# Performance work log

Hardware: AMD Instinct MI355X
Metric: run time of the kernel (lower is better)

Reference implementation:

```python
import jax, jax.numpy as jnp
import numpy as np

VOCAB, EMB, HID, B, T = 32000, 256, 256, 64, 2048


def setup_inputs() -> dict:
    key = jax.random.key(0)
    ks = jax.random.split(key, 6)
    s = 1.0 / np.sqrt(HID)
    return {
        "source": jax.random.randint(ks[0], (B, T), 0, VOCAB),
        "embedding": jax.random.normal(ks[1], (VOCAB, EMB), dtype=jnp.float32) * 0.02,
        "W_ih": jax.random.uniform(ks[2], (EMB, HID), jnp.float32, -s, s),
        "W_hh": jax.random.uniform(ks[3], (HID, HID), jnp.float32, -s, s),
        "b_ih": jax.random.uniform(ks[4], (HID,), jnp.float32, -s, s),
        "b_hh": jax.random.uniform(ks[5], (HID,), jnp.float32, -s, s),
    }


def reference(source, embedding, W_ih, W_hh, b_ih, b_hh):
    # embedding lookup: [B, T, EMB]
    embedded = embedding[source]
    # scan over time with carried hidden state (RNNCellManual: tanh cell)
    xs = jnp.swapaxes(embedded, 0, 1)  # [T, B, EMB]

    def step(h, x_t):
        h_new = jnp.tanh(x_t @ W_ih + b_ih + h @ W_hh + b_hh)
        return h_new, None

    h0 = jnp.zeros((source.shape[0], W_hh.shape[0]), dtype=embedding.dtype)
    h_T, _ = jax.lax.scan(step, h0, xs)
    return h_T  # final hidden state [B, HID]
```

## Files before the change

### kernel.cpp

```cpp
#include <hip/hip_runtime.h>

#define TT 2048
#define BB 64
#define HH 256

typedef _Float16 half2_t __attribute__((ext_vector_type(2)));
typedef _Float16 half8_t __attribute__((ext_vector_type(8)));
typedef float f32x4 __attribute__((ext_vector_type(4)));
typedef int i32x4 __attribute__((ext_vector_type(4)));

__global__ void prep_kernel(const float* __restrict__ Wih, const float* __restrict__ Whh,
                            _Float16* __restrict__ WihT, _Float16* __restrict__ WhhT) {
  const int n = blockIdx.x;
  const int k = threadIdx.x;
  WihT[n * HH + k] = (_Float16)Wih[k * HH + n];
  WhhT[n * HH + k] = (_Float16)Whh[k * HH + n];
}

__global__ __launch_bounds__(256, 2) void embed_gemm_kernel(
    const int* __restrict__ source, const float* __restrict__ emb,
    const _Float16* __restrict__ WihT, const float* __restrict__ b_ih,
    const float* __restrict__ b_hh, _Float16* __restrict__ U) {
  const int t = blockIdx.x;
  const int nbase = blockIdx.y * 64;
  __shared__ __align__(16) _Float16 Bs[64][280];

  const int tid = threadIdx.x;
  for (int c = tid; c < 64 * 32; c += 256) {
    const int n = c >> 5;
    const int ko = (c & 31) * 8;
    *(half8_t*)&Bs[n][ko] = *(const half8_t*)(WihT + (size_t)(nbase + n) * HH + ko);
  }
  __syncthreads();

  const int lane = tid & 63;
  const int wave = tid >> 6;
  const int row16 = lane & 15;
  const int quad = lane >> 4;
  const int b = wave * 16 + row16;
  const int src = source[b * TT + t];
  const float* arow = emb + (size_t)src * HH + quad * 8;

  f32x4 acc[4];
#pragma unroll
  for (int ct = 0; ct < 4; ++ct) acc[ct] = (f32x4){0.f, 0.f, 0.f, 0.f};

#pragma unroll
  for (int kt = 0; kt < 8; ++kt) {
    const float4 x0 = *(const float4*)(arow + kt * 32);
    const float4 x1 = *(const float4*)(arow + kt * 32 + 4);
    half8_t af;
    af[0] = (_Float16)x0.x; af[1] = (_Float16)x0.y;
    af[2] = (_Float16)x0.z; af[3] = (_Float16)x0.w;
    af[4] = (_Float16)x1.x; af[5] = (_Float16)x1.y;
    af[6] = (_Float16)x1.z; af[7] = (_Float16)x1.w;
#pragma unroll
    for (int ct = 0; ct < 4; ++ct) {
      const half8_t bf = *(const half8_t*)&Bs[ct * 16 + row16][quad * 8 + kt * 32];
      acc[ct] = __builtin_amdgcn_mfma_f32_16x16x32_f16(af, bf, acc[ct], 0, 0, 0);
    }
  }

#pragma unroll
  for (int ct = 0; ct < 4; ++ct) {
    const int nn = nbase + ct * 16 + row16;
    const float bias = b_ih[nn] + b_hh[nn];
#pragma unroll
    for (int r = 0; r < 4; ++r) {
      const int bb = wave * 16 + quad * 4 + r;
      U[((size_t)t * BB + bb) * HH + nn] = (_Float16)(acc[ct][r] + bias);
    }
  }
}

__global__ __launch_bounds__(256)
__attribute__((amdgpu_waves_per_eu(1, 1)))
void rnn_scan_kernel(
    const _Float16* __restrict__ U, const _Float16* __restrict__ WhhT,
    float* __restrict__ out) {
  const int b = blockIdx.x;
  const int tid = threadIdx.x;
  const int w = tid >> 6;
  const int l = tid & 63;
  const int col = l & 15;
  const int quad = l >> 4;

  __shared__ __align__(16) _Float16 hbuf[2][HH];

  half8_t wb[4][8];
#pragma unroll
  for (int tt = 0; tt < 4; ++tt) {
    const _Float16* base = WhhT + (size_t)(64 * w + 16 * tt + col) * HH + quad * 8;
#pragma unroll
    for (int c = 0; c < 8; ++c) wb[tt][c] = *(const half8_t*)(base + 32 * c);
  }
  asm volatile("" : "+a"(wb[0][0]), "+a"(wb[0][1]), "+a"(wb[0][2]), "+a"(wb[0][3]),
                    "+a"(wb[0][4]), "+a"(wb[0][5]), "+a"(wb[0][6]), "+a"(wb[0][7]),
                    "+a"(wb[1][0]), "+a"(wb[1][1]), "+a"(wb[1][2]), "+a"(wb[1][3]),
                    "+a"(wb[1][4]), "+a"(wb[1][5]), "+a"(wb[1][6]), "+a"(wb[1][7]));
  asm volatile("" : "+a"(wb[2][0]), "+a"(wb[2][1]), "+a"(wb[2][2]), "+a"(wb[2][3]),
                    "+a"(wb[2][4]), "+a"(wb[2][5]), "+a"(wb[2][6]), "+a"(wb[2][7]),
                    "+a"(wb[3][0]), "+a"(wb[3][1]), "+a"(wb[3][2]), "+a"(wb[3][3]),
                    "+a"(wb[3][4]), "+a"(wb[3][5]), "+a"(wb[3][6]), "+a"(wb[3][7]));

  hbuf[0][tid] = (_Float16)0.f;

  const _Float16* Up = U + b * HH + tid;
  _Float16 uc[8], un[8];
#pragma unroll
  for (int s = 0; s < 8; ++s) uc[s] = Up[(size_t)s * (BB * HH)];

  float hn = 0.f;
  __syncthreads();

  for (int tc = 0; tc < TT; tc += 8) {
    const int tn = (tc + 8) & (TT - 1);
#pragma unroll
    for (int s = 0; s < 8; ++s) un[s] = Up[(size_t)(tn + s) * (BB * HH)];

#pragma unroll
    for (int s = 0; s < 8; ++s) {
      const int t = tc + s;

      const _Float16* hrow = hbuf[t & 1] + quad * 8;
      half8_t ha[8];
#pragma unroll
      for (int c = 0; c < 8; ++c) ha[c] = *(const half8_t*)(hrow + 32 * c);
      asm volatile("" : "+v"(ha[0]), "+v"(ha[1]), "+v"(ha[2]), "+v"(ha[3]),
                        "+v"(ha[4]), "+v"(ha[5]), "+v"(ha[6]), "+v"(ha[7]));

      f32x4 cacc[4];
#pragma unroll
      for (int tt = 0; tt < 4; ++tt) cacc[tt] = (f32x4){0.f, 0.f, 0.f, 0.f};
#pragma unroll
      for (int c = 0; c < 8; ++c)
#pragma unroll
        for (int tt = 0; tt < 4; ++tt)
          cacc[tt] = __builtin_amdgcn_mfma_f32_16x16x32_f16(ha[c], wb[tt][c], cacc[tt], 0, 0, 0);

      float y = cacc[0][0];
      y = (quad == 1) ? cacc[1][0] : y;
      y = (quad == 2) ? cacc[2][0] : y;
      y = (quad == 3) ? cacc[3][0] : y;

      const float a = (float)uc[s] + y;
      const float e = __builtin_amdgcn_exp2f(a * 2.885390081777927f);
      hn = 1.f - 2.f * __builtin_amdgcn_rcpf(e + 1.f);
      hbuf[(t + 1) & 1][tid] = (_Float16)hn;

      __syncthreads();
    }
#pragma unroll
    for (int s = 0; s < 8; ++s) uc[s] = un[s];
  }
  out[(size_t)b * HH + tid] = hn;
}

extern "C" void kernel_launch(void* const* d_in, const int* in_sizes, int n_in,
                              void* d_out, int out_size, void* d_ws, size_t ws_size,
                              hipStream_t stream) {
  const int*   source = (const int*)d_in[0];
  const float* emb    = (const float*)d_in[1];
  const float* Wih    = (const float*)d_in[2];
  const float* Whh    = (const float*)d_in[3];
  const float* bih    = (const float*)d_in[4];
  const float* bhh    = (const float*)d_in[5];
  float* out = (float*)d_out;

  char* ws = (char*)d_ws;
  _Float16* U    = (_Float16*)ws;
  _Float16* WihT = (_Float16*)(ws + 67108864);
  _Float16* WhhT = (_Float16*)(ws + 67239936);

  prep_kernel<<<dim3(256), dim3(256), 0, stream>>>(Wih, Whh, WihT, WhhT);
  embed_gemm_kernel<<<dim3(TT, 4), dim3(256), 0, stream>>>(source, emb, WihT, bih, bhh, U);
  rnn_scan_kernel<<<dim3(BB), dim3(256), 0, stream>>>(U, WhhT, out);
}
```

Baseline: 946.6 us.

## Start own-wave hidden-state MFMAs before barrier in RNN scan

Each wave's columns of W_hh are permuted so its first two K-chunks line up with the hidden-state slice that the same wave just wrote. Those two chunks are read from LDS and their MFMAs issued right after the tanh, before the block barrier. The other six chunks run after an explicit waitcnt plus s_barrier. The aim is to shorten the serial critical path of each timestep by overlapping a quarter of the recurrent matmul with barrier latency. The risk is that correctness depends on the inline-asm barrier and on intra-wave LDS ordering, and the floating-point summation order changes.

New measurement: 914.3 us. -3.4%, faster.

```diff
diff --git a/kernel.cpp b/kernel.cpp
--- a/kernel.cpp
+++ b/kernel.cpp
@@ -7,7 +7,6 @@
 typedef _Float16 half2_t __attribute__((ext_vector_type(2)));
 typedef _Float16 half8_t __attribute__((ext_vector_type(8)));
 typedef float f32x4 __attribute__((ext_vector_type(4)));
-typedef int i32x4 __attribute__((ext_vector_type(4)));
 
 __global__ void prep_kernel(const float* __restrict__ Wih, const float* __restrict__ Whh,
                             _Float16* __restrict__ WihT, _Float16* __restrict__ WhhT) {
@@ -92,7 +91,10 @@
   for (int tt = 0; tt < 4; ++tt) {
     const _Float16* base = WhhT + (size_t)(64 * w + 16 * tt + col) * HH + quad * 8;
 #pragma unroll
-    for (int c = 0; c < 8; ++c) wb[tt][c] = *(const half8_t*)(base + 32 * c);
+    for (int j = 0; j < 8; ++j) {
+      const int c = (2 * w + j) & 7;
+      wb[tt][j] = *(const half8_t*)(base + 32 * c);
+    }
   }
   asm volatile("" : "+a"(wb[0][0]), "+a"(wb[0][1]), "+a"(wb[0][2]), "+a"(wb[0][3]),
                     "+a"(wb[0][4]), "+a"(wb[0][5]), "+a"(wb[0][6]), "+a"(wb[0][7]),
@@ -103,6 +105,15 @@
                     "+a"(wb[3][0]), "+a"(wb[3][1]), "+a"(wb[3][2]), "+a"(wb[3][3]),
                     "+a"(wb[3][4]), "+a"(wb[3][5]), "+a"(wb[3][6]), "+a"(wb[3][7]));
 
+  const int oO0 = 32 * ((2 * w + 0) & 7) + 8 * quad;
+  const int oO1 = 32 * ((2 * w + 1) & 7) + 8 * quad;
+  const int oX2 = 32 * ((2 * w + 2) & 7) + 8 * quad;
+  const int oX3 = 32 * ((2 * w + 3) & 7) + 8 * quad;
+  const int oX4 = 32 * ((2 * w + 4) & 7) + 8 * quad;
+  const int oX5 = 32 * ((2 * w + 5) & 7) + 8 * quad;
+  const int oX6 = 32 * ((2 * w + 6) & 7) + 8 * quad;
+  const int oX7 = 32 * ((2 * w + 7) & 7) + 8 * quad;
+
   hbuf[0][tid] = (_Float16)0.f;
 
   const _Float16* Up = U + b * HH + tid;
@@ -111,7 +122,21 @@
   for (int s = 0; s < 8; ++s) uc[s] = Up[(size_t)s * (BB * HH)];
 
   float hn = 0.f;
-  __syncthreads();
+  f32x4 cacc[4];
+#pragma unroll
+  for (int tt = 0; tt < 4; ++tt) cacc[tt] = (f32x4){0.f, 0.f, 0.f, 0.f};
+
+  {
+    half8_t hoA = *(const half8_t*)(hbuf[0] + oO0);
+    half8_t hoB = *(const half8_t*)(hbuf[0] + oO1);
+    asm volatile("" : "+v"(hoA), "+v"(hoB));
+#pragma unroll
+    for (int tt = 0; tt < 4; ++tt)
+      cacc[tt] = __builtin_amdgcn_mfma_f32_16x16x32_f16(hoA, wb[tt][0], cacc[tt], 0, 0, 0);
+#pragma unroll
+    for (int tt = 0; tt < 4; ++tt)
+      cacc[tt] = __builtin_amdgcn_mfma_f32_16x16x32_f16(hoB, wb[tt][1], cacc[tt], 0, 0, 0);
+  }
 
   for (int tc = 0; tc < TT; tc += 8) {
     const int tn = (tc + 8) & (TT - 1);
@@ -122,21 +147,35 @@
     for (int s = 0; s < 8; ++s) {
       const int t = tc + s;
 
-      const _Float16* hrow = hbuf[t & 1] + quad * 8;
-      half8_t ha[8];
-#pragma unroll
-      for (int c = 0; c < 8; ++c) ha[c] = *(const half8_t*)(hrow + 32 * c);
-      asm volatile("" : "+v"(ha[0]), "+v"(ha[1]), "+v"(ha[2]), "+v"(ha[3]),
-                        "+v"(ha[4]), "+v"(ha[5]), "+v"(ha[6]), "+v"(ha[7]));
-
-      f32x4 cacc[4];
-#pragma unroll
-      for (int tt = 0; tt < 4; ++tt) cacc[tt] = (f32x4){0.f, 0.f, 0.f, 0.f};
-#pragma unroll
-      for (int c = 0; c < 8; ++c)
-#pragma unroll
-        for (int tt = 0; tt < 4; ++tt)
-          cacc[tt] = __builtin_amdgcn_mfma_f32_16x16x32_f16(ha[c], wb[tt][c], cacc[tt], 0, 0, 0);
+      asm volatile("s_waitcnt lgkmcnt(0)\n\ts_barrier" ::: "memory");
+
+      const _Float16* hb = hbuf[t & 1];
+      half8_t h2 = *(const half8_t*)(hb + oX2);
+      half8_t h3 = *(const half8_t*)(hb + oX3);
+      half8_t h4 = *(const half8_t*)(hb + oX4);
+      half8_t h5 = *(const half8_t*)(hb + oX5);
+      half8_t h6 = *(const half8_t*)(hb + oX6);
+      half8_t h7 = *(const half8_t*)(hb + oX7);
+      asm volatile("" : "+v"(h2), "+v"(h3), "+v"(h4), "+v"(h5), "+v"(h6), "+v"(h7));
+
+#pragma unroll
+      for (int tt = 0; tt < 4; ++tt)
+        cacc[tt] = __builtin_amdgcn_mfma_f32_16x16x32_f16(h2, wb[tt][2], cacc[tt], 0, 0, 0);
+#pragma unroll
+      for (int tt = 0; tt < 4; ++tt)
+        cacc[tt] = __builtin_amdgcn_mfma_f32_16x16x32_f16(h3, wb[tt][3], cacc[tt], 0, 0, 0);
+#pragma unroll
+      for (int tt = 0; tt < 4; ++tt)
+        cacc[tt] = __builtin_amdgcn_mfma_f32_16x16x32_f16(h4, wb[tt][4], cacc[tt], 0, 0, 0);
+#pragma unroll
+      for (int tt = 0; tt < 4; ++tt)
+        cacc[tt] = __builtin_amdgcn_mfma_f32_16x16x32_f16(h5, wb[tt][5], cacc[tt], 0, 0, 0);
+#pragma unroll
+      for (int tt = 0; tt < 4; ++tt)
+        cacc[tt] = __builtin_amdgcn_mfma_f32_16x16x32_f16(h6, wb[tt][6], cacc[tt], 0, 0, 0);
+#pragma unroll
+      for (int tt = 0; tt < 4; ++tt)
+        cacc[tt] = __builtin_amdgcn_mfma_f32_16x16x32_f16(h7, wb[tt][7], cacc[tt], 0, 0, 0);
 
       float y = cacc[0][0];
       y = (quad == 1) ? cacc[1][0] : y;
@@ -146,9 +185,20 @@
       const float a = (float)uc[s] + y;
       const float e = __builtin_amdgcn_exp2f(a * 2.885390081777927f);
       hn = 1.f - 2.f * __builtin_amdgcn_rcpf(e + 1.f);
-      hbuf[(t + 1) & 1][tid] = (_Float16)hn;
-
-      __syncthreads();
+
+      _Float16* hb1 = (_Float16*)hbuf[(t + 1) & 1];
+      hb1[tid] = (_Float16)hn;
+      half8_t hoA = *(const half8_t*)(hb1 + oO0);
+      half8_t hoB = *(const half8_t*)(hb1 + oO1);
+      asm volatile("" : "+v"(hoA), "+v"(hoB));
+#pragma unroll
+      for (int tt = 0; tt < 4; ++tt) cacc[tt] = (f32x4){0.f, 0.f, 0.f, 0.f};
+#pragma unroll
+      for (int tt = 0; tt < 4; ++tt)
+        cacc[tt] = __builtin_amdgcn_mfma_f32_16x16x32_f16(hoA, wb[tt][0], cacc[tt], 0, 0, 0);
+#pragma unroll
+      for (int tt = 0; tt < 4; ++tt)
+        cacc[tt] = __builtin_amdgcn_mfma_f32_16x16x32_f16(hoB, wb[tt][1], cacc[tt], 0, 0, 0);
     }
 #pragma unroll
     for (int s = 0; s < 8; ++s) uc[s] = un[s];
```
